# Kernel optimization log

Hardware: AMD Instinct MI355X
Metric: run time of the kernel (lower is better)

The kernel has to match this reference:

```python
import math
import jax, jax.numpy as jnp
import numpy as np

jax.config.update("jax_enable_x64", True)  # hash math uses int64, as in the torch reference

N_LEVELS = 16
F = 2                     # n_feat_per_entry
T = 2 ** 19               # hashmap size per level (max)
BASE_RES = 16
MAX_RES = 512
MIN_XYZ = -0.75           # origin (0,0,0), side 1.5
MAX_XYZ = 0.75
B = 1_000_000

# per_level_scale computed in float32 like torch.exp(torch.log(...))
_SCALE = float(np.exp(np.log(np.float32(MAX_RES / BASE_RES)) / np.float32(N_LEVELS - 1)))

def _level_info():
    offsets, res, n = [], [], 0
    for i in range(N_LEVELS):
        offsets.append(n)
        r = math.floor(BASE_RES * _SCALE ** i)
        res.append(r)
        n += min(T, (r + 1) ** 3)
    offsets.append(n)
    return offsets, res, n

OFFSETS, RES, N_TOTAL = _level_info()  # N_TOTAL == 5262476
PRIMES = np.array([1, 2654435761, 805459861], dtype=np.int64)
# corner offsets in {0,1}^3; weight = prod over dims of (frac if corner==1 else 1-frac)
CORNERS = np.array([[i, j, k] for i in (0, 1) for j in (0, 1) for k in (0, 1)], dtype=np.int64)  # (8,3)


def _hashgrid_forward(xyz, embeddings):
    """xyz: (B,3) float32 inside the bbox; embeddings: (N_TOTAL,F) float32."""
    norm = (xyz - MIN_XYZ) / (MAX_XYZ - MIN_XYZ)  # (B,3) in [0,1]
    corners = jnp.asarray(CORNERS)                # (8,3) int64
    primes = jnp.asarray(PRIMES)                  # (3,) int64
    corner_is_one = jnp.asarray(CORNERS.astype(bool))  # (8,3)
    outs = [xyz]  # include_input=True, raw input first
    for lvl in range(N_LEVELS):
        r = RES[lvl]
        off = OFFSETS[lvl]
        size = OFFSETS[lvl + 1] - off   # = min(T, (r+1)^3)
        pos = norm * r                                     # (B,3)
        base = jnp.clip(jnp.floor(pos).astype(jnp.int64), 0, r - 1)  # (B,3)
        frac = pos - base.astype(pos.dtype)                # (B,3)
        idx3 = base[:, None, :] + corners[None]            # (B,8,3) grid-pt coords
        # fast_hash: xor of coord*prime per dim, then mod level size, plus level offset
        p = idx3 * primes                                  # (B,8,3) int64
        hidx = (p[..., 0] ^ p[..., 1] ^ p[..., 2]) % size + off  # (B,8)
        vals = embeddings[hidx]                            # (B,8,F) gather
        w = jnp.prod(jnp.where(corner_is_one[None], frac[:, None, :], 1.0 - frac[:, None, :]), axis=-1)  # (B,8)
        outs.append(jnp.einsum('bc,bcf->bf', w, vals))     # trilinear interp -> (B,F)
    return jnp.concatenate(outs, axis=-1)                  # (B, 3 + L*F) = (B,35)


def setup_inputs() -> dict:
    key = jax.random.key(0)
    k1, k2 = jax.random.split(key)
    # points strictly inside the bbox [-0.75, 0.75]^3
    xyz = jax.random.uniform(k1, (B, 3), dtype=jnp.float32,
                             minval=MIN_XYZ + 1e-3, maxval=MAX_XYZ - 1e-3)
    # torch init is uniform(-1e-4, 1e-4)
    emb = jax.random.uniform(k2, (N_TOTAL, F), dtype=jnp.float32, minval=-1e-4, maxval=1e-4)
    return {"xyz": xyz, "embeddings": emb}


def reference(xyz, embeddings):
    return _hashgrid_forward(xyz, embeddings)
```

## Files before the change

kernel.cpp:

```cpp
#include <hip/hip_runtime.h>
#include <stdint.h>
#include <string.h>

#define NLEV 16

__device__ __forceinline__ void norm_coords(const float* __restrict__ xyz, int p,
                                            float& nx, float& ny, float& nz) {
    const float x = __builtin_nontemporal_load(xyz + 3 * p + 0);
    const float y = __builtin_nontemporal_load(xyz + 3 * p + 1);
    const float z = __builtin_nontemporal_load(xyz + 3 * p + 2);
    const float inv = 1.0f / 1.5f;
    nx = (x + 0.75f) * inv;
    ny = (y + 0.75f) * inv;
    nz = (z + 0.75f) * inv;
}

template<int R>
__device__ __forceinline__ void big_prep(float nx, float ny, float nz,
                                         uint32_t h[8],
                                         float& fx, float& fy, float& fz) {
    const float rf = (float)R;
    const float px = nx * rf, py = ny * rf, pz = nz * rf;
    int bx = (int)floorf(px); bx = bx < 0 ? 0 : (bx > R - 1 ? R - 1 : bx);
    int by = (int)floorf(py); by = by < 0 ? 0 : (by > R - 1 ? R - 1 : by);
    int bz = (int)floorf(pz); bz = bz < 0 ? 0 : (bz > R - 1 ? R - 1 : bz);
    fx = px - (float)bx;
    fy = py - (float)by;
    fz = pz - (float)bz;

    const uint32_t M = 524287u;
    const uint32_t hx0 = (uint32_t)bx;
    const uint32_t hx1 = hx0 + 1u;
    const uint32_t hy0 = (uint32_t)by       * 2654435761u;
    const uint32_t hy1 = (uint32_t)(by + 1) * 2654435761u;
    const uint32_t hz0 = (uint32_t)bz       * 805459861u;
    const uint32_t hz1 = (uint32_t)(bz + 1) * 805459861u;

    const uint32_t yz00 = hy0 ^ hz0, yz01 = hy0 ^ hz1;
    const uint32_t yz10 = hy1 ^ hz0, yz11 = hy1 ^ hz1;

    h[0] = (hx0 ^ yz00) & M;
    h[1] = (hx0 ^ yz01) & M;
    h[2] = (hx0 ^ yz10) & M;
    h[3] = (hx0 ^ yz11) & M;
    h[4] = (hx1 ^ yz00) & M;
    h[5] = (hx1 ^ yz01) & M;
    h[6] = (hx1 ^ yz10) & M;
    h[7] = (hx1 ^ yz11) & M;
}

__device__ __forceinline__ float2 trilerp(const float2 v[8],
                                          float fx, float fy, float fz) {
    const float gx = 1.0f - fx, gy = 1.0f - fy, gz = 1.0f - fz;
    const float w00 = gx * gy, w01 = gx * fy, w10 = fx * gy, w11 = fx * fy;
    float w, f0, f1;
    w = w00 * gz; f0 = w * v[0].x;          f1 = w * v[0].y;
    w = w00 * fz; f0 = fmaf(w, v[1].x, f0); f1 = fmaf(w, v[1].y, f1);
    w = w01 * gz; f0 = fmaf(w, v[2].x, f0); f1 = fmaf(w, v[2].y, f1);
    w = w01 * fz; f0 = fmaf(w, v[3].x, f0); f1 = fmaf(w, v[3].y, f1);
    w = w10 * gz; f0 = fmaf(w, v[4].x, f0); f1 = fmaf(w, v[4].y, f1);
    w = w10 * fz; f0 = fmaf(w, v[5].x, f0); f1 = fmaf(w, v[5].y, f1);
    w = w11 * gz; f0 = fmaf(w, v[6].x, f0); f1 = fmaf(w, v[6].y, f1);
    w = w11 * fz; f0 = fmaf(w, v[7].x, f0); f1 = fmaf(w, v[7].y, f1);
    return make_float2(f0, f1);
}

template<int R, uint32_t OFF>
__global__ __launch_bounds__(256, 4) void big_level2(
    const float* __restrict__ xyz,
    const float2* __restrict__ emb,
    float2* __restrict__ ws,
    int nb)
{
    const int t  = threadIdx.x;
    const int p0 = blockIdx.x * 512 + t;
    const int p1 = p0 + 256;
    const int q0 = p0 < nb ? p0 : nb - 1;
    const int q1 = p1 < nb ? p1 : nb - 1;

    float nxA, nyA, nzA, nxB, nyB, nzB;
    norm_coords(xyz, q0, nxA, nyA, nzA);
    norm_coords(xyz, q1, nxB, nyB, nzB);

    uint32_t hA[8], hB[8];
    float fxA, fyA, fzA, fxB, fyB, fzB;
    big_prep<R>(nxA, nyA, nzA, hA, fxA, fyA, fzA);
    big_prep<R>(nxB, nyB, nzB, hB, fxB, fyB, fzB);

    float2 vA[8], vB[8];
    #pragma unroll
    for (int c = 0; c < 8; ++c) vA[c] = emb[hA[c] + OFF];
    #pragma unroll
    for (int c = 0; c < 8; ++c) vB[c] = emb[hB[c] + OFF];

    const float2 rA = trilerp(vA, fxA, fyA, fzA);
    const float2 rB = trilerp(vB, fxB, fyB, fzB);

    uint64_t uA, uB;
    memcpy(&uA, &rA, 8);
    memcpy(&uB, &rB, 8);
    if (p0 < nb) __builtin_nontemporal_store(uA, (uint64_t*)ws + p0);
    if (p1 < nb) __builtin_nontemporal_store(uB, (uint64_t*)ws + p1);
}

__global__ __launch_bounds__(256, 4) void pack_small(
    const float* __restrict__ xyz,
    const float2* __restrict__ emb,
    const float2* __restrict__ ws,
    float* __restrict__ out,
    int nb)
{
    constexpr int      kRes[7]  = {16, 20, 25, 32, 40, 50, 64};
    constexpr uint32_t kSize[7] = {4913u, 9261u, 17576u, 35937u, 68921u, 132651u, 274625u};
    constexpr uint32_t kOff[7]  = {0u, 4913u, 14174u, 31750u, 67687u, 136608u, 269259u};

    __shared__ __align__(16) float lds[4 * 64 * 35];

    const int tid  = threadIdx.x;
    const int lane = tid & 63;
    const int wid  = tid >> 6;
    const int p    = blockIdx.x * 256 + tid;
    const int pc   = (p < nb) ? p : (nb - 1);

    uint64_t wsv[9];
    #pragma unroll
    for (int l = 0; l < 9; ++l)
        wsv[l] = __builtin_nontemporal_load(
            (const uint64_t*)ws + (size_t)l * nb + pc);

    const float x = xyz[3 * pc + 0];
    const float y = xyz[3 * pc + 1];
    const float z = xyz[3 * pc + 2];

    float* wl = &lds[(wid * 64 + lane) * 35];
    wl[0] = x; wl[1] = y; wl[2] = z;

    const float inv = 1.0f / 1.5f;
    const float nx = (x + 0.75f) * inv;
    const float ny = (y + 0.75f) * inv;
    const float nz = (z + 0.75f) * inv;

    #pragma unroll
    for (int l = 0; l < 7; ++l) {
        const int      r   = kRes[l];
        const float    rf  = (float)r;
        const uint32_t sz  = kSize[l];
        const uint32_t off = kOff[l];

        const float px = nx * rf, py = ny * rf, pz = nz * rf;
        int bx = (int)floorf(px); bx = bx < 0 ? 0 : (bx > r - 1 ? r - 1 : bx);
        int by = (int)floorf(py); by = by < 0 ? 0 : (by > r - 1 ? r - 1 : by);
        int bz = (int)floorf(pz); bz = bz < 0 ? 0 : (bz > r - 1 ? r - 1 : bz);
        const float fx = px - (float)bx;
        const float fy = py - (float)by;
        const float fz = pz - (float)bz;

        const uint64_t hx0 = (uint64_t)(uint32_t)bx;
        const uint64_t hx1 = hx0 + 1u;
        const uint64_t hy0 = (uint64_t)(uint32_t)by       * 2654435761ull;
        const uint64_t hy1 = (uint64_t)(uint32_t)(by + 1) * 2654435761ull;
        const uint64_t hz0 = (uint64_t)(uint32_t)bz       * 805459861ull;
        const uint64_t hz1 = (uint64_t)(uint32_t)(bz + 1) * 805459861ull;

        const uint64_t yz00 = hy0 ^ hz0, yz01 = hy0 ^ hz1;
        const uint64_t yz10 = hy1 ^ hz0, yz11 = hy1 ^ hz1;

        const uint32_t i000 = (uint32_t)((hx0 ^ yz00) % sz) + off;
        const uint32_t i001 = (uint32_t)((hx0 ^ yz01) % sz) + off;
        const uint32_t i010 = (uint32_t)((hx0 ^ yz10) % sz) + off;
        const uint32_t i011 = (uint32_t)((hx0 ^ yz11) % sz) + off;
        const uint32_t i100 = (uint32_t)((hx1 ^ yz00) % sz) + off;
        const uint32_t i101 = (uint32_t)((hx1 ^ yz01) % sz) + off;
        const uint32_t i110 = (uint32_t)((hx1 ^ yz10) % sz) + off;
        const uint32_t i111 = (uint32_t)((hx1 ^ yz11) % sz) + off;

        const float2 v000 = emb[i000];
        const float2 v001 = emb[i001];
        const float2 v010 = emb[i010];
        const float2 v011 = emb[i011];
        const float2 v100 = emb[i100];
        const float2 v101 = emb[i101];
        const float2 v110 = emb[i110];
        const float2 v111 = emb[i111];

        const float gx = 1.0f - fx, gy = 1.0f - fy, gz = 1.0f - fz;
        const float w00 = gx * gy, w01 = gx * fy, w10 = fx * gy, w11 = fx * fy;

        float w, f0, f1;
        w = w00 * gz; f0 = w * v000.x;          f1 = w * v000.y;
        w = w00 * fz; f0 = fmaf(w, v001.x, f0); f1 = fmaf(w, v001.y, f1);
        w = w01 * gz; f0 = fmaf(w, v010.x, f0); f1 = fmaf(w, v010.y, f1);
        w = w01 * fz; f0 = fmaf(w, v011.x, f0); f1 = fmaf(w, v011.y, f1);
        w = w10 * gz; f0 = fmaf(w, v100.x, f0); f1 = fmaf(w, v100.y, f1);
        w = w10 * fz; f0 = fmaf(w, v101.x, f0); f1 = fmaf(w, v101.y, f1);
        w = w11 * gz; f0 = fmaf(w, v110.x, f0); f1 = fmaf(w, v110.y, f1);
        w = w11 * fz; f0 = fmaf(w, v111.x, f0); f1 = fmaf(w, v111.y, f1);

        wl[3 + 2 * l] = f0;
        wl[4 + 2 * l] = f1;
    }

    #pragma unroll
    for (int l = 0; l < 9; ++l) {
        float2 v;
        memcpy(&v, &wsv[l], 8);
        wl[3 + 2 * (l + 7)] = v.x;
        wl[4 + 2 * (l + 7)] = v.y;
    }

    __syncthreads();

    const int wave_gid = blockIdx.x * 4 + wid;
    if (wave_gid * 64 < nb) {
        const float4* s4 = (const float4*)&lds[wid * 64 * 35];
        float4* d4 = (float4*)(out + (size_t)wave_gid * (64 * 35));
        #pragma unroll
        for (int c = 0; c < 8; ++c)
            d4[c * 64 + lane] = s4[c * 64 + lane];
        if (lane < 48)
            d4[8 * 64 + lane] = s4[8 * 64 + lane];
    }
}

__global__ __launch_bounds__(256, 4) void hashgrid_mono(
    const float* __restrict__ xyz,
    const float2* __restrict__ emb,
    float* __restrict__ out,
    int nb)
{
    constexpr int      kRes[NLEV]  = {16,20,25,32,40,50,64,80,101,128,161,203,256,322,406,512};
    constexpr uint32_t kSize[NLEV] = {4913u,9261u,17576u,35937u,68921u,132651u,274625u,
                                      524288u,524288u,524288u,524288u,524288u,
                                      524288u,524288u,524288u,524288u};
    constexpr uint32_t kOff[NLEV]  = {0u,4913u,14174u,31750u,67687u,136608u,269259u,543884u,
                                      1068172u,1592460u,2116748u,2641036u,3165324u,
                                      3689612u,4213900u,4738188u};

    __shared__ __align__(16) float lds[4 * 64 * 35];

    const int tid  = threadIdx.x;
    const int lane = tid & 63;
    const int wid  = tid >> 6;
    const int p    = blockIdx.x * 256 + tid;
    const int pc   = (p < nb) ? p : (nb - 1);

    const float x = xyz[3 * pc + 0];
    const float y = xyz[3 * pc + 1];
    const float z = xyz[3 * pc + 2];

    float* wl = &lds[(wid * 64 + lane) * 35];
    wl[0] = x; wl[1] = y; wl[2] = z;

    const float inv = 1.0f / 1.5f;
    const float nx = (x + 0.75f) * inv;
    const float ny = (y + 0.75f) * inv;
    const float nz = (z + 0.75f) * inv;

    #pragma unroll
    for (int l = 0; l < NLEV; ++l) {
        const int      r   = kRes[l];
        const float    rf  = (float)r;
        const uint32_t sz  = kSize[l];
        const uint32_t off = kOff[l];

        const float px = nx * rf, py = ny * rf, pz = nz * rf;
        int bx = (int)floorf(px); bx = bx < 0 ? 0 : (bx > r - 1 ? r - 1 : bx);
        int by = (int)floorf(py); by = by < 0 ? 0 : (by > r - 1 ? r - 1 : by);
        int bz = (int)floorf(pz); bz = bz < 0 ? 0 : (bz > r - 1 ? r - 1 : bz);
        const float fx = px - (float)bx;
        const float fy = py - (float)by;
        const float fz = pz - (float)bz;

        const uint64_t hx0 = (uint64_t)(uint32_t)bx;
        const uint64_t hx1 = hx0 + 1u;
        const uint64_t hy0 = (uint64_t)(uint32_t)by       * 2654435761ull;
        const uint64_t hy1 = (uint64_t)(uint32_t)(by + 1) * 2654435761ull;
        const uint64_t hz0 = (uint64_t)(uint32_t)bz       * 805459861ull;
        const uint64_t hz1 = (uint64_t)(uint32_t)(bz + 1) * 805459861ull;

        const uint64_t yz00 = hy0 ^ hz0, yz01 = hy0 ^ hz1;
        const uint64_t yz10 = hy1 ^ hz0, yz11 = hy1 ^ hz1;

        const uint32_t i000 = (uint32_t)((hx0 ^ yz00) % sz) + off;
        const uint32_t i001 = (uint32_t)((hx0 ^ yz01) % sz) + off;
        const uint32_t i010 = (uint32_t)((hx0 ^ yz10) % sz) + off;
        const uint32_t i011 = (uint32_t)((hx0 ^ yz11) % sz) + off;
        const uint32_t i100 = (uint32_t)((hx1 ^ yz00) % sz) + off;
        const uint32_t i101 = (uint32_t)((hx1 ^ yz01) % sz) + off;
        const uint32_t i110 = (uint32_t)((hx1 ^ yz10) % sz) + off;
        const uint32_t i111 = (uint32_t)((hx1 ^ yz11) % sz) + off;

        const float2 v000 = emb[i000];
        const float2 v001 = emb[i001];
        const float2 v010 = emb[i010];
        const float2 v011 = emb[i011];
        const float2 v100 = emb[i100];
        const float2 v101 = emb[i101];
        const float2 v110 = emb[i110];
        const float2 v111 = emb[i111];

        const float gx = 1.0f - fx, gy = 1.0f - fy, gz = 1.0f - fz;
        const float w00 = gx * gy, w01 = gx * fy, w10 = fx * gy, w11 = fx * fy;

        float w, f0, f1;
        w = w00 * gz; f0 = w * v000.x;          f1 = w * v000.y;
        w = w00 * fz; f0 = fmaf(w, v001.x, f0); f1 = fmaf(w, v001.y, f1);
        w = w01 * gz; f0 = fmaf(w, v010.x, f0); f1 = fmaf(w, v010.y, f1);
        w = w01 * fz; f0 = fmaf(w, v011.x, f0); f1 = fmaf(w, v011.y, f1);
        w = w10 * gz; f0 = fmaf(w, v100.x, f0); f1 = fmaf(w, v100.y, f1);
        w = w10 * fz; f0 = fmaf(w, v101.x, f0); f1 = fmaf(w, v101.y, f1);
        w = w11 * gz; f0 = fmaf(w, v110.x, f0); f1 = fmaf(w, v110.y, f1);
        w = w11 * fz; f0 = fmaf(w, v111.x, f0); f1 = fmaf(w, v111.y, f1);

        wl[3 + 2 * l] = f0;
        wl[4 + 2 * l] = f1;
    }

    __syncthreads();

    const int wave_gid = blockIdx.x * 4 + wid;
    if (wave_gid * 64 < nb) {
        const float* src = &lds[wid * 64 * 35];
        float* dst = out + (size_t)wave_gid * (64 * 35);
        #pragma unroll
        for (int c = 0; c < 35; ++c)
            dst[c * 64 + lane] = src[c * 64 + lane];
    }
}

extern "C" void kernel_launch(void* const* d_in, const int* in_sizes, int n_in,
                              void* d_out, int out_size, void* d_ws, size_t ws_size,
                              hipStream_t stream) {
    const float*  xyz = (const float*)d_in[0];
    const float2* emb = (const float2*)d_in[1];
    float*        out = (float*)d_out;
    const int nb = in_sizes[0] / 3;
    const int blocks  = (nb + 255) / 256;
    const int blocks2 = (nb + 511) / 512;

    const size_t ws_need = (size_t)9 * (size_t)nb * sizeof(float2);
    if (ws_size < ws_need) {
        hashgrid_mono<<<blocks, 256, 0, stream>>>(xyz, emb, out, nb);
        return;
    }

    float2* ws = (float2*)d_ws;
    big_level2< 80,  543884u><<<blocks2, 256, 0, stream>>>(xyz, emb, ws + (size_t)0 * nb, nb);
    big_level2<101, 1068172u><<<blocks2, 256, 0, stream>>>(xyz, emb, ws + (size_t)1 * nb, nb);
    big_level2<128, 1592460u><<<blocks2, 256, 0, stream>>>(xyz, emb, ws + (size_t)2 * nb, nb);
    big_level2<161, 2116748u><<<blocks2, 256, 0, stream>>>(xyz, emb, ws + (size_t)3 * nb, nb);
    big_level2<203, 2641036u><<<blocks2, 256, 0, stream>>>(xyz, emb, ws + (size_t)4 * nb, nb);
    big_level2<256, 3165324u><<<blocks2, 256, 0, stream>>>(xyz, emb, ws + (size_t)5 * nb, nb);
    big_level2<322, 3689612u><<<blocks2, 256, 0, stream>>>(xyz, emb, ws + (size_t)6 * nb, nb);
    big_level2<406, 4213900u><<<blocks2, 256, 0, stream>>>(xyz, emb, ws + (size_t)7 * nb, nb);
    big_level2<512, 4738188u><<<blocks2, 256, 0, stream>>>(xyz, emb, ws + (size_t)8 * nb, nb);
    pack_small<<<blocks, 256, 0, stream>>>(xyz, emb, ws, out, nb);
}
```

Measured before the change: 721.5 us.

## Pair adjacent-x corner gathers into float4 loads and pipeline small-level gathers

In the big-level kernel, the x0 and x0+1 corners hash to adjacent table entries when bx is even, because with prime 1 on x only the low bit differs. Those two corners are now fetched with a single 16-byte load, and the extra four 8-byte loads are issued only when bx is odd. The small-level packer issues the gathers for the next level before interpolating the current one, to overlap memory latency. It also switches the final output copy to nontemporal stores. This costs extra registers and adds divergence between lanes with odd and even bx.

```diff
diff --git a/kernel.cpp b/kernel.cpp
--- a/kernel.cpp
+++ b/kernel.cpp
@@ -3,6 +3,8 @@
 #include <string.h>
 
 #define NLEV 16
+
+typedef float  vfloat4 __attribute__((ext_vector_type(4)));
 
 __device__ __forceinline__ void norm_coords(const float* __restrict__ xyz, int p,
                                             float& nx, float& ny, float& nz) {
@@ -13,40 +15,6 @@
     nx = (x + 0.75f) * inv;
     ny = (y + 0.75f) * inv;
     nz = (z + 0.75f) * inv;
-}
-
-template<int R>
-__device__ __forceinline__ void big_prep(float nx, float ny, float nz,
-                                         uint32_t h[8],
-                                         float& fx, float& fy, float& fz) {
-    const float rf = (float)R;
-    const float px = nx * rf, py = ny * rf, pz = nz * rf;
-    int bx = (int)floorf(px); bx = bx < 0 ? 0 : (bx > R - 1 ? R - 1 : bx);
-    int by = (int)floorf(py); by = by < 0 ? 0 : (by > R - 1 ? R - 1 : by);
-    int bz = (int)floorf(pz); bz = bz < 0 ? 0 : (bz > R - 1 ? R - 1 : bz);
-    fx = px - (float)bx;
-    fy = py - (float)by;
-    fz = pz - (float)bz;
-
-    const uint32_t M = 524287u;
-    const uint32_t hx0 = (uint32_t)bx;
-    const uint32_t hx1 = hx0 + 1u;
-    const uint32_t hy0 = (uint32_t)by       * 2654435761u;
-    const uint32_t hy1 = (uint32_t)(by + 1) * 2654435761u;
-    const uint32_t hz0 = (uint32_t)bz       * 805459861u;
-    const uint32_t hz1 = (uint32_t)(bz + 1) * 805459861u;
-
-    const uint32_t yz00 = hy0 ^ hz0, yz01 = hy0 ^ hz1;
-    const uint32_t yz10 = hy1 ^ hz0, yz11 = hy1 ^ hz1;
-
-    h[0] = (hx0 ^ yz00) & M;
-    h[1] = (hx0 ^ yz01) & M;
-    h[2] = (hx0 ^ yz10) & M;
-    h[3] = (hx0 ^ yz11) & M;
-    h[4] = (hx1 ^ yz00) & M;
-    h[5] = (hx1 ^ yz01) & M;
-    h[6] = (hx1 ^ yz10) & M;
-    h[7] = (hx1 ^ yz11) & M;
 }
 
 __device__ __forceinline__ float2 trilerp(const float2 v[8],
@@ -75,32 +43,79 @@
     const int t  = threadIdx.x;
     const int p0 = blockIdx.x * 512 + t;
     const int p1 = p0 + 256;
-    const int q0 = p0 < nb ? p0 : nb - 1;
-    const int q1 = p1 < nb ? p1 : nb - 1;
-
-    float nxA, nyA, nzA, nxB, nyB, nzB;
-    norm_coords(xyz, q0, nxA, nyA, nzA);
-    norm_coords(xyz, q1, nxB, nyB, nzB);
-
-    uint32_t hA[8], hB[8];
-    float fxA, fyA, fzA, fxB, fyB, fzB;
-    big_prep<R>(nxA, nyA, nzA, hA, fxA, fyA, fzA);
-    big_prep<R>(nxB, nyB, nzB, hB, fxB, fyB, fzB);
-
-    float2 vA[8], vB[8];
-    #pragma unroll
-    for (int c = 0; c < 8; ++c) vA[c] = emb[hA[c] + OFF];
-    #pragma unroll
-    for (int c = 0; c < 8; ++c) vB[c] = emb[hB[c] + OFF];
-
-    const float2 rA = trilerp(vA, fxA, fyA, fzA);
-    const float2 rB = trilerp(vB, fxB, fyB, fzB);
-
-    uint64_t uA, uB;
-    memcpy(&uA, &rA, 8);
-    memcpy(&uB, &rB, 8);
-    if (p0 < nb) __builtin_nontemporal_store(uA, (uint64_t*)ws + p0);
-    if (p1 < nb) __builtin_nontemporal_store(uB, (uint64_t*)ws + p1);
+    const int q[2] = { p0 < nb ? p0 : nb - 1, p1 < nb ? p1 : nb - 1 };
+
+    const float4* __restrict__ emb4 = (const float4*)emb;
+    const uint32_t M = 524287u;
+
+    uint32_t h0[2][4];
+    uint32_t yzs[2][4];
+    uint32_t hx1_[2];
+    float4   V[2][4];
+    float2   w1[2][4];
+    float    fx[2], fy[2], fz[2];
+    bool     oddbx[2];
+
+    #pragma unroll
+    for (int j = 0; j < 2; ++j) {
+        float nx, ny, nz;
+        norm_coords(xyz, q[j], nx, ny, nz);
+        const float rf = (float)R;
+        const float px = nx * rf, py = ny * rf, pz = nz * rf;
+        int bx = (int)floorf(px); bx = bx < 0 ? 0 : (bx > R - 1 ? R - 1 : bx);
+        int by = (int)floorf(py); by = by < 0 ? 0 : (by > R - 1 ? R - 1 : by);
+        int bz = (int)floorf(pz); bz = bz < 0 ? 0 : (bz > R - 1 ? R - 1 : bz);
+        fx[j] = px - (float)bx;
+        fy[j] = py - (float)by;
+        fz[j] = pz - (float)bz;
+
+        const uint32_t hy0 = (uint32_t)by       * 2654435761u;
+        const uint32_t hy1 = (uint32_t)(by + 1) * 2654435761u;
+        const uint32_t hz0 = (uint32_t)bz       * 805459861u;
+        const uint32_t hz1 = (uint32_t)(bz + 1) * 805459861u;
+        yzs[j][0] = hy0 ^ hz0; yzs[j][1] = hy0 ^ hz1;
+        yzs[j][2] = hy1 ^ hz0; yzs[j][3] = hy1 ^ hz1;
+
+        const uint32_t hx0 = (uint32_t)bx;
+        oddbx[j] = (bx & 1) != 0;
+        hx1_[j]  = hx0 + 1u;
+
+        #pragma unroll
+        for (int i = 0; i < 4; ++i) {
+            h0[j][i] = (hx0 ^ yzs[j][i]) & M;
+            V[j][i]  = emb4[(h0[j][i] >> 1) + (OFF >> 1)];
+        }
+    }
+
+    #pragma unroll
+    for (int j = 0; j < 2; ++j) {
+        if (oddbx[j]) {
+            #pragma unroll
+            for (int i = 0; i < 4; ++i)
+                w1[j][i] = emb[((hx1_[j] ^ yzs[j][i]) & M) + OFF];
+        }
+    }
+
+    float2 r[2];
+    #pragma unroll
+    for (int j = 0; j < 2; ++j) {
+        float2 v[8];
+        #pragma unroll
+        for (int i = 0; i < 4; ++i) {
+            const float2 lo = make_float2(V[j][i].x, V[j][i].y);
+            const float2 hi = make_float2(V[j][i].z, V[j][i].w);
+            const bool oh = (h0[j][i] & 1u) != 0u;
+            v[i]     = oh ? hi : lo;
+            v[i + 4] = oddbx[j] ? w1[j][i] : (oh ? lo : hi);
+        }
+        r[j] = trilerp(v, fx[j], fy[j], fz[j]);
+    }
+
+    uint64_t u0, u1;
+    memcpy(&u0, &r[0], 8);
+    memcpy(&u1, &r[1], 8);
+    if (p0 < nb) __builtin_nontemporal_store(u0, (uint64_t*)ws + p0);
+    if (p1 < nb) __builtin_nontemporal_store(u1, (uint64_t*)ws + p1);
 }
 
 __global__ __launch_bounds__(256, 4) void pack_small(
@@ -140,20 +155,23 @@
     const float ny = (y + 0.75f) * inv;
     const float nz = (z + 0.75f) * inv;
 
-    #pragma unroll
-    for (int l = 0; l < 7; ++l) {
-        const int      r   = kRes[l];
+    uint32_t idx[2][8];
+    float2   v[2][8];
+    float    fr[2][3];
+
+    auto level_idx = [&](int lv, uint32_t (&ix)[8], float (&f)[3]) {
+        const int      r   = kRes[lv];
         const float    rf  = (float)r;
-        const uint32_t sz  = kSize[l];
-        const uint32_t off = kOff[l];
+        const uint32_t sz  = kSize[lv];
+        const uint32_t off = kOff[lv];
 
         const float px = nx * rf, py = ny * rf, pz = nz * rf;
         int bx = (int)floorf(px); bx = bx < 0 ? 0 : (bx > r - 1 ? r - 1 : bx);
         int by = (int)floorf(py); by = by < 0 ? 0 : (by > r - 1 ? r - 1 : by);
         int bz = (int)floorf(pz); bz = bz < 0 ? 0 : (bz > r - 1 ? r - 1 : bz);
-        const float fx = px - (float)bx;
-        const float fy = py - (float)by;
-        const float fz = pz - (float)bz;
+        f[0] = px - (float)bx;
+        f[1] = py - (float)by;
+        f[2] = pz - (float)bz;
 
         const uint64_t hx0 = (uint64_t)(uint32_t)bx;
         const uint64_t hx1 = hx0 + 1u;
@@ -165,60 +183,53 @@
         const uint64_t yz00 = hy0 ^ hz0, yz01 = hy0 ^ hz1;
         const uint64_t yz10 = hy1 ^ hz0, yz11 = hy1 ^ hz1;
 
-        const uint32_t i000 = (uint32_t)((hx0 ^ yz00) % sz) + off;
-        const uint32_t i001 = (uint32_t)((hx0 ^ yz01) % sz) + off;
-        const uint32_t i010 = (uint32_t)((hx0 ^ yz10) % sz) + off;
-        const uint32_t i011 = (uint32_t)((hx0 ^ yz11) % sz) + off;
-        const uint32_t i100 = (uint32_t)((hx1 ^ yz00) % sz) + off;
-        const uint32_t i101 = (uint32_t)((hx1 ^ yz01) % sz) + off;
-        const uint32_t i110 = (uint32_t)((hx1 ^ yz10) % sz) + off;
-        const uint32_t i111 = (uint32_t)((hx1 ^ yz11) % sz) + off;
-
-        const float2 v000 = emb[i000];
-        const float2 v001 = emb[i001];
-        const float2 v010 = emb[i010];
-        const float2 v011 = emb[i011];
-        const float2 v100 = emb[i100];
-        const float2 v101 = emb[i101];
-        const float2 v110 = emb[i110];
-        const float2 v111 = emb[i111];
-
-        const float gx = 1.0f - fx, gy = 1.0f - fy, gz = 1.0f - fz;
-        const float w00 = gx * gy, w01 = gx * fy, w10 = fx * gy, w11 = fx * fy;
-
-        float w, f0, f1;
-        w = w00 * gz; f0 = w * v000.x;          f1 = w * v000.y;
-        w = w00 * fz; f0 = fmaf(w, v001.x, f0); f1 = fmaf(w, v001.y, f1);
-        w = w01 * gz; f0 = fmaf(w, v010.x, f0); f1 = fmaf(w, v010.y, f1);
-        w = w01 * fz; f0 = fmaf(w, v011.x, f0); f1 = fmaf(w, v011.y, f1);
-        w = w10 * gz; f0 = fmaf(w, v100.x, f0); f1 = fmaf(w, v100.y, f1);
-        w = w10 * fz; f0 = fmaf(w, v101.x, f0); f1 = fmaf(w, v101.y, f1);
-        w = w11 * gz; f0 = fmaf(w, v110.x, f0); f1 = fmaf(w, v110.y, f1);
-        w = w11 * fz; f0 = fmaf(w, v111.x, f0); f1 = fmaf(w, v111.y, f1);
-
-        wl[3 + 2 * l] = f0;
-        wl[4 + 2 * l] = f1;
+        ix[0] = (uint32_t)((hx0 ^ yz00) % sz) + off;
+        ix[1] = (uint32_t)((hx0 ^ yz01) % sz) + off;
+        ix[2] = (uint32_t)((hx0 ^ yz10) % sz) + off;
+        ix[3] = (uint32_t)((hx0 ^ yz11) % sz) + off;
+        ix[4] = (uint32_t)((hx1 ^ yz00) % sz) + off;
+        ix[5] = (uint32_t)((hx1 ^ yz01) % sz) + off;
+        ix[6] = (uint32_t)((hx1 ^ yz10) % sz) + off;
+        ix[7] = (uint32_t)((hx1 ^ yz11) % sz) + off;
+    };
+
+    level_idx(0, idx[0], fr[0]);
+    #pragma unroll
+    for (int i = 0; i < 8; ++i) v[0][i] = emb[idx[0][i]];
+
+    #pragma unroll
+    for (int l = 0; l < 7; ++l) {
+        const int cur = l & 1;
+        const int nxt = cur ^ 1;
+        if (l < 6) {
+            level_idx(l + 1, idx[nxt], fr[nxt]);
+            #pragma unroll
+            for (int i = 0; i < 8; ++i) v[nxt][i] = emb[idx[nxt][i]];
+        }
+        const float2 rr = trilerp(v[cur], fr[cur][0], fr[cur][1], fr[cur][2]);
+        wl[3 + 2 * l] = rr.x;
+        wl[4 + 2 * l] = rr.y;
     }
 
     #pragma unroll
     for (int l = 0; l < 9; ++l) {
-        float2 v;
-        memcpy(&v, &wsv[l], 8);
-        wl[3 + 2 * (l + 7)] = v.x;
-        wl[4 + 2 * (l + 7)] = v.y;
+        float2 bv;
+        memcpy(&bv, &wsv[l], 8);
+        wl[3 + 2 * (l + 7)] = bv.x;
+        wl[4 + 2 * (l + 7)] = bv.y;
     }
 
     __syncthreads();
 
     const int wave_gid = blockIdx.x * 4 + wid;
     if (wave_gid * 64 < nb) {
-        const float4* s4 = (const float4*)&lds[wid * 64 * 35];
-        float4* d4 = (float4*)(out + (size_t)wave_gid * (64 * 35));
+        const vfloat4* s4 = (const vfloat4*)&lds[wid * 64 * 35];
+        vfloat4* d4 = (vfloat4*)(out + (size_t)wave_gid * (64 * 35));
         #pragma unroll
         for (int c = 0; c < 8; ++c)
-            d4[c * 64 + lane] = s4[c * 64 + lane];
+            __builtin_nontemporal_store(s4[c * 64 + lane], &d4[c * 64 + lane]);
         if (lane < 48)
-            d4[8 * 64 + lane] = s4[8 * 64 + lane];
+            __builtin_nontemporal_store(s4[8 * 64 + lane], &d4[8 * 64 + lane]);
     }
 }
 
```

Result: faster. 625.2 us (-13.3%).
